# Optimization experiments

Measured on AMD Instinct MI355X. Metric: run time of the kernel, lower is better.

The kernel has to match this reference:

```python
import jax, jax.numpy as jnp
import numpy as np

NUM_USERS = 100000
USER_EMB_DIM = 64
PROC_DIM = 128          # Dense(128) embedding_processor
NUM_SHARDS = 16
MEM_SIZE = 512          # memory slots per shard
WORD_SIZE = 64
NUM_READS = 4
INPUT_SIZE = 256
B, S = 256, 128
IN_DIM = INPUT_SIZE + PROC_DIM  # combined controller input width


def setup_inputs() -> dict:
    key = jax.random.key(0)
    k = jax.random.split(key, 7)
    x = jax.random.normal(k[0], (B, S, INPUT_SIZE), dtype=jnp.float32)
    user_id = jax.random.randint(k[1], (B,), 0, NUM_USERS, dtype=jnp.int64)
    user_emb_table = jax.random.normal(k[2], (NUM_USERS, USER_EMB_DIM), dtype=jnp.float32) * 0.02
    W_proc = jax.random.normal(k[3], (USER_EMB_DIM, PROC_DIM), dtype=jnp.float32) * (1.0 / np.sqrt(USER_EMB_DIM))
    b_proc = jnp.zeros((PROC_DIM,), dtype=jnp.float32)
    # per-shard parameters: query projection + memory matrix (the shard's state)
    Wq = jax.random.normal(k[4], (NUM_SHARDS, IN_DIM, NUM_READS * WORD_SIZE), dtype=jnp.float32) * (1.0 / np.sqrt(IN_DIM))
    memory = jax.random.normal(k[5], (NUM_SHARDS, MEM_SIZE, WORD_SIZE), dtype=jnp.float32)
    return {"x": x, "user_id": user_id, "user_emb_table": user_emb_table,
            "W_proc": W_proc, "b_proc": b_proc, "Wq": Wq, "memory": memory}


def reference(x, user_id, user_emb_table, W_proc, b_proc, Wq, memory):
    # user embedding lookup + Dense processor
    ue = user_emb_table[user_id]                       # [B, E]
    pe = ue @ W_proc + b_proc                          # [B, PROC_DIM]
    # broadcast the processed embedding across the sequence and concat on features
    pe_seq = jnp.broadcast_to(pe[:, None, :], (x.shape[0], x.shape[1], pe.shape[-1]))
    combined = jnp.concatenate([x, pe_seq], axis=-1)   # [B, S, IN_DIM]
    # shard routing (irregular gather of per-shard params)
    sid = user_id % NUM_SHARDS                         # [B]
    Wq_g = Wq[sid]                                     # [B, IN_DIM, R*W]
    mem_g = memory[sid]                                # [B, M, W]
    # per-sample shard forward: content-based read
    q = jnp.einsum('bsi,bio->bso', combined, Wq_g)     # [B, S, R*W]
    q = q.reshape(q.shape[0], q.shape[1], NUM_READS, WORD_SIZE)
    scores = jnp.einsum('bsrw,bmw->bsrm', q, mem_g)    # [B, S, R, M]
    wts = jax.nn.softmax(scores, axis=-1)
    read_words = jnp.einsum('bsrm,bmw->bsrw', wts, mem_g)  # [B, S, R, W]
    # original code keeps final_states[-1] (last sample's state)
    final_state = wts[-1]                              # [S, R, M]
    return read_words, final_state
```

## Files before the change

### kernel.cpp

```cpp
#include <hip/hip_runtime.h>
#include <math.h>

#define BB 256
#define SSEQ 128
#define INPUT 256
#define PD 128
#define EE 64
#define RW 256
#define MM 512
#define WW 64
#define KD 384

typedef _Float16 half8 __attribute__((ext_vector_type(8)));
typedef __fp16 fp16x2 __attribute__((ext_vector_type(2)));
typedef float float4v __attribute__((ext_vector_type(4)));
typedef float f32x16 __attribute__((ext_vector_type(16)));
typedef unsigned int uint2v __attribute__((ext_vector_type(2)));

#define LOG2E 1.44269504088896f
#define OUT1 8388608u

#define MEMT_OFF 65536
#define MEMT16   4096
#define F32_OFF  131072
#define LDS_BYTES (131072 + 6144)
#define UE_O 0
#define PE_O 64
#define QPE_O 192
#define QP_O 448

union H8 { half8 h8; unsigned int u[4]; uint4 u4; };

__device__ __forceinline__ unsigned int pk2(float a, float b) {
    union { fp16x2 h; unsigned int u; } p;
    p.h = __builtin_amdgcn_cvt_pkrtz(a, b);
    return p.u;
}

__device__ __forceinline__ float xhalf_max(float v) {
    uint2v r = __builtin_amdgcn_permlane32_swap(__float_as_uint(v), __float_as_uint(v), false, false);
    return fmaxf(__uint_as_float(r[0]), __uint_as_float(r[1]));
}
__device__ __forceinline__ float xhalf_sum(float v) {
    uint2v r = __builtin_amdgcn_permlane32_swap(__float_as_uint(v), __float_as_uint(v), false, false);
    return __uint_as_float(r[0]) + __uint_as_float(r[1]);
}

__global__ void __launch_bounds__(1024, 4)
attn_kernel(const float* __restrict__ x, const int* __restrict__ user_id,
            const float* __restrict__ uet, const float* __restrict__ W_proc,
            const float* __restrict__ b_proc, const float* __restrict__ Wq,
            const float* __restrict__ memG, float* __restrict__ out)
{
    extern __shared__ char smraw[];
    unsigned short* smemu = (unsigned short*)smraw;
    unsigned int*   smw   = (unsigned int*)smraw;
    uint4*          sm128 = (uint4*)smraw;
    float*          smf   = (float*)(smraw + F32_OFF);

    const int t = threadIdx.x;
    const int b = blockIdx.x;
    const int lane = t & 63, wv = t >> 6;
    const int n16 = lane & 15, quad = lane >> 4;
    const int l31 = lane & 31, hh = lane >> 5;
    const int r = wv & 3, sq = wv >> 2;
    const int s0 = sq * 32;
    const int mswz = l31 & 7;

    const int uid = user_id[b];
    const int sid = uid & 15;
    const float* memB = memG + (size_t)sid * (MM*WW);
    const float* wqX  = Wq + (size_t)sid * KD * RW;

    if (t < EE) smf[UE_O + t] = uet[(size_t)uid*EE + t];

    for (int i = 0; i < 32; ++i) {
        int idx = i*1024 + t;
        int n = idx & 255, kp = idx >> 8;
        float w0 = wqX[(size_t)(2*kp)    *RW + n];
        float w1 = wqX[(size_t)(2*kp + 1)*RW + n];
        smw[((((kp>>2)*256 + n) << 2) | (kp & 3))] = pk2(w0, w1);
    }
    __syncthreads();

    if (t < PD) {
        float a = b_proc[t];
        #pragma unroll
        for (int e = 0; e < EE; ++e) a = fmaf(smf[UE_O + e], W_proc[e*PD + t], a);
        smf[PE_O + t] = a;
    }
    __syncthreads();
    {
        int n = t & 255, h = t >> 8;
        float s = 0.f;
        const float* wr = wqX + (size_t)(256 + h*32)*RW + n;
        #pragma unroll 8
        for (int k = 0; k < 32; ++k) s = fmaf(smf[PE_O + h*32 + k], wr[(size_t)k*RW], s);
        smf[QP_O + h*256 + n] = s;
    }
    __syncthreads();
    if (t < 256) smf[QPE_O + t] = LOG2E * (smf[QP_O + t] + smf[QP_O + 256 + t]
                                         + smf[QP_O + 512 + t] + smf[QP_O + 768 + t]);
    __syncthreads();

    float4v qacc[4][2];
    #pragma unroll
    for (int mt = 0; mt < 4; ++mt)
        #pragma unroll
        for (int nt = 0; nt < 2; ++nt) qacc[mt][nt] = (float4v)0.f;

    const float* xB = x + (size_t)(b*SSEQ + s0) * INPUT;
    for (int kc = 0; kc < 8; ++kc) {
        H8 afr[4];
        #pragma unroll
        for (int mt = 0; mt < 4; ++mt)
            afr[mt].u4 = sm128[(kc*4 + quad)*256 + r*64 + mt*16 + n16];
        H8 bfr[2];
        #pragma unroll
        for (int nt = 0; nt < 2; ++nt) {
            const float* xg = xB + (size_t)(nt*16 + n16)*INPUT + kc*32 + quad*8;
            float4 a0 = *(const float4*)xg;
            float4 a1 = *(const float4*)(xg + 4);
            bfr[nt].u[0] = pk2(a0.x*LOG2E, a0.y*LOG2E);
            bfr[nt].u[1] = pk2(a0.z*LOG2E, a0.w*LOG2E);
            bfr[nt].u[2] = pk2(a1.x*LOG2E, a1.y*LOG2E);
            bfr[nt].u[3] = pk2(a1.z*LOG2E, a1.w*LOG2E);
        }
        __builtin_amdgcn_s_setprio(1);
        #pragma unroll
        for (int mt = 0; mt < 4; ++mt)
            #pragma unroll
            for (int nt = 0; nt < 2; ++nt)
                qacc[mt][nt] = __builtin_amdgcn_mfma_f32_16x16x32_f16(afr[mt].h8, bfr[nt].h8, qacc[mt][nt], 0, 0, 0);
        __builtin_amdgcn_s_setprio(0);
    }
    #pragma unroll
    for (int mt = 0; mt < 4; ++mt)
        #pragma unroll
        for (int reg = 0; reg < 4; ++reg) {
            float qv = smf[QPE_O + r*64 + mt*16 + quad*4 + reg];
            #pragma unroll
            for (int nt = 0; nt < 2; ++nt) qacc[mt][nt][reg] += qv;
        }
    unsigned int pkq[4][2][2];
    #pragma unroll
    for (int mt = 0; mt < 4; ++mt)
        #pragma unroll
        for (int nt = 0; nt < 2; ++nt) {
            pkq[mt][nt][0] = pk2(qacc[mt][nt][0], qacc[mt][nt][1]);
            pkq[mt][nt][1] = pk2(qacc[mt][nt][2], qacc[mt][nt][3]);
        }
    H8 bqf[4];
    {
        const int ntSel = (lane >> 4) & 1;
        const int srcBase = (lane & 15) + (lane & 32);
        #pragma unroll
        for (int kc = 0; kc < 4; ++kc)
            #pragma unroll
            for (int jp = 0; jp < 4; ++jp) {
                const int src = srcBase + ((jp >> 1) << 4);
                int v0 = __shfl((int)pkq[kc][0][jp & 1], src, 64);
                int v1 = __shfl((int)pkq[kc][1][jp & 1], src, 64);
                bqf[kc].u[jp] = (unsigned int)(ntSel ? v1 : v0);
            }
    }
    __syncthreads();

    for (int i = 0; i < 4; ++i) {
        int id = t + i*1024;
        int m = id >> 3, cw = id & 7;
        const float* g = memB + m*64 + cw*8;
        float4 a0 = *(const float4*)g;
        float4 a1 = *(const float4*)(g + 4);
        sm128[m*8 + (cw ^ (m & 7))] =
            make_uint4(pk2(a0.x,a0.y), pk2(a0.z,a0.w), pk2(a1.x,a1.y), pk2(a1.z,a1.w));
    }
    __syncthreads();
    for (int i = 0; i < 4; ++i) {
        int id = t + i*1024;
        int w = id & 63, cm = id >> 6;
        unsigned int uu[4];
        #pragma unroll
        for (int p = 0; p < 4; ++p) {
            int m0 = cm*8 + 2*p, m1 = m0 + 1;
            unsigned short lo = smemu[m0*64 + (((w>>3) ^ (m0&7))<<3) + (w&7)];
            unsigned short hi = smemu[m1*64 + (((w>>3) ^ (m1&7))<<3) + (w&7)];
            uu[p] = (unsigned int)lo | ((unsigned int)hi << 16);
        }
        sm128[MEMT16 + w*64 + (cm ^ (w & 7))] = make_uint4(uu[0],uu[1],uu[2],uu[3]);
    }
    __syncthreads();

    f32x16 Oa0 = (f32x16)0.f, Oa1 = (f32x16)0.f;
    float Ml = -1e30f, llp = 0.f;

    H8 afc[4];
    #pragma unroll
    for (int kc = 0; kc < 4; ++kc)
        afc[kc].u4 = sm128[l31*8 + (((kc<<1) + hh) ^ mswz)];

    for (int mtile = 0; mtile < 16; ++mtile) {
        f32x16 Sa = (f32x16)0.f;
        __builtin_amdgcn_s_setprio(1);
        #pragma unroll
        for (int kc = 0; kc < 4; ++kc)
            Sa = __builtin_amdgcn_mfma_f32_32x32x16_f16(afc[kc].h8, bqf[kc].h8, Sa, 0, 0, 0);
        __builtin_amdgcn_s_setprio(0);
        if (mtile < 15) {
            const int mrow = (mtile+1)*32 + l31;
            #pragma unroll
            for (int kc = 0; kc < 4; ++kc)
                afc[kc].u4 = sm128[mrow*8 + (((kc<<1) + hh) ^ mswz)];
        }
        const int c0 = mtile*4 + hh;
        H8 afP0, afP1, afP2, afP3;
        afP0.u4 = sm128[MEMT16 + l31*64        + ( c0      ^ mswz)];
        afP1.u4 = sm128[MEMT16 + l31*64        + ((c0 + 2) ^ mswz)];
        afP2.u4 = sm128[MEMT16 + (32 + l31)*64 + ( c0      ^ mswz)];
        afP3.u4 = sm128[MEMT16 + (32 + l31)*64 + ((c0 + 2) ^ mswz)];
        float m0 = fmaxf(fmaxf(Sa[0], Sa[1]), Sa[2]);
        float m1 = fmaxf(fmaxf(Sa[3], Sa[4]), Sa[5]);
        float m2 = fmaxf(fmaxf(Sa[6], Sa[7]), Sa[8]);
        float m3 = fmaxf(fmaxf(Sa[9], Sa[10]), Sa[11]);
        float m4 = fmaxf(fmaxf(Sa[12], Sa[13]), Sa[14]);
        float m5 = fmaxf(fmaxf(m0, m1), Sa[15]);
        float m6 = fmaxf(fmaxf(m2, m3), m4);
        float tmx = xhalf_max(fmaxf(m5, m6));
        if (__any(tmx > Ml + 8.0f)) {
            float Mn = fmaxf(Ml, tmx);
            float al = __builtin_amdgcn_exp2f(Ml - Mn);
            Ml = Mn;
            llp *= al;
            #pragma unroll
            for (int g = 0; g < 16; ++g) { Oa0[g] *= al; Oa1[g] *= al; }
        }
        float pv[16];
        #pragma unroll
        for (int g = 0; g < 16; ++g) pv[g] = __builtin_amdgcn_exp2f(Sa[g] - Ml);
        float ts = (((pv[0]+pv[1])+(pv[2]+pv[3])) + ((pv[4]+pv[5])+(pv[6]+pv[7])))
                 + (((pv[8]+pv[9])+(pv[10]+pv[11])) + ((pv[12]+pv[13])+(pv[14]+pv[15])));
        llp += ts;
        uint2v rA0 = __builtin_amdgcn_permlane32_swap(pk2(pv[0],pv[1]),   pk2(pv[4],pv[5]),   false, false);
        uint2v rB0 = __builtin_amdgcn_permlane32_swap(pk2(pv[2],pv[3]),   pk2(pv[6],pv[7]),   false, false);
        uint2v rA1 = __builtin_amdgcn_permlane32_swap(pk2(pv[8],pv[9]),   pk2(pv[12],pv[13]), false, false);
        uint2v rB1 = __builtin_amdgcn_permlane32_swap(pk2(pv[10],pv[11]), pk2(pv[14],pv[15]), false, false);
        H8 bp0; bp0.u[0]=rA0[0]; bp0.u[1]=rB0[0]; bp0.u[2]=rA0[1]; bp0.u[3]=rB0[1];
        H8 bp1; bp1.u[0]=rA1[0]; bp1.u[1]=rB1[0]; bp1.u[2]=rA1[1]; bp1.u[3]=rB1[1];
        __builtin_amdgcn_s_setprio(1);
        Oa0 = __builtin_amdgcn_mfma_f32_32x32x16_f16(afP0.h8, bp0.h8, Oa0, 0, 0, 0);
        Oa0 = __builtin_amdgcn_mfma_f32_32x32x16_f16(afP1.h8, bp1.h8, Oa0, 0, 0, 0);
        Oa1 = __builtin_amdgcn_mfma_f32_32x32x16_f16(afP2.h8, bp0.h8, Oa1, 0, 0, 0);
        Oa1 = __builtin_amdgcn_mfma_f32_32x32x16_f16(afP3.h8, bp1.h8, Oa1, 0, 0, 0);
        __builtin_amdgcn_s_setprio(0);
    }

    float inv = 1.0f / xhalf_sum(llp);

    {
        const int s = s0 + l31;
        float* op = out + ((size_t)(b*SSEQ + s)*4 + r)*WW;
        #pragma unroll
        for (int rq = 0; rq < 4; ++rq) {
            float4 o0 = make_float4(Oa0[rq*4+0]*inv, Oa0[rq*4+1]*inv,
                                    Oa0[rq*4+2]*inv, Oa0[rq*4+3]*inv);
            *(float4*)&op[rq*8 + hh*4] = o0;
            float4 o1 = make_float4(Oa1[rq*4+0]*inv, Oa1[rq*4+1]*inv,
                                    Oa1[rq*4+2]*inv, Oa1[rq*4+3]*inv);
            *(float4*)&op[32 + rq*8 + hh*4] = o1;
        }
    }

    if (b == BB - 1) {
        const int s = s0 + l31;
        size_t base = (size_t)OUT1 + ((size_t)(s*4 + r) << 9);
        for (int mtile = 0; mtile < 16; ++mtile) {
            f32x16 Sa = (f32x16)0.f;
            const int mrow = mtile*32 + l31;
            #pragma unroll
            for (int kc = 0; kc < 4; ++kc) {
                H8 af; af.u4 = sm128[mrow*8 + (((kc<<1) + hh) ^ mswz)];
                Sa = __builtin_amdgcn_mfma_f32_32x32x16_f16(af.h8, bqf[kc].h8, Sa, 0, 0, 0);
            }
            #pragma unroll
            for (int rq = 0; rq < 4; ++rq) {
                float4 w4 = make_float4(
                    __builtin_amdgcn_exp2f(Sa[rq*4+0] - Ml) * inv,
                    __builtin_amdgcn_exp2f(Sa[rq*4+1] - Ml) * inv,
                    __builtin_amdgcn_exp2f(Sa[rq*4+2] - Ml) * inv,
                    __builtin_amdgcn_exp2f(Sa[rq*4+3] - Ml) * inv);
                *(float4*)&out[base + mtile*32 + rq*8 + hh*4] = w4;
            }
        }
    }
}

extern "C" void kernel_launch(void* const* d_in, const int* in_sizes, int n_in,
                              void* d_out, int out_size, void* d_ws, size_t ws_size,
                              hipStream_t stream) {
    const float* x    = (const float*)d_in[0];
    const int*   uid  = (const int*)  d_in[1];
    const float* uet  = (const float*)d_in[2];
    const float* Wp   = (const float*)d_in[3];
    const float* bp   = (const float*)d_in[4];
    const float* Wq   = (const float*)d_in[5];
    const float* mem  = (const float*)d_in[6];
    float* out = (float*)d_out;

    (void)hipFuncSetAttribute((const void*)attn_kernel,
                              hipFuncAttributeMaxDynamicSharedMemorySize, LDS_BYTES);
    attn_kernel<<<BB, 1024, LDS_BYTES, stream>>>(x, uid, uet, Wp, bp, Wq, mem, out);
}
```

Before: 165.8 us.

## Split attention into prep, query-projection and attention kernels via workspace

Adds a prep kernel that converts each shard's memory to fp16 once, in both row-major and transposed form, in global workspace. The former single kernel is split in two. The first computes the query fragments and writes them to global memory. The second loads the precomputed fp16 memory tiles directly into LDS, removing the per-block fp32 convert and LDS transpose passes and their barriers. The trade-off is two extra launches and a global round-trip of the query fragments, and it needs enough workspace, otherwise the original monolithic kernel is used.

```diff
diff --git a/kernel.cpp b/kernel.cpp
--- a/kernel.cpp
+++ b/kernel.cpp
@@ -23,12 +23,20 @@
 #define MEMT_OFF 65536
 #define MEMT16   4096
 #define F32_OFF  131072
-#define LDS_BYTES (131072 + 6144)
+#define LDS_BYTES_K1 (131072 + 6144)
+#define LDS_BYTES_K2 131072
 #define UE_O 0
 #define PE_O 64
 #define QPE_O 192
 #define QP_O 448
 
+#define QG_OFF   0u
+#define M16_OFF  (16u<<20)
+#define MT16_OFF (17u<<20)
+#define WS_NEED  (18u<<20)
+
+#define QIDX(b,r,kc,jp,hh,s) ((((((size_t)(b)*4 + (r))*4 + (kc))*4 + (jp))*2 + (hh))*128 + (s))
+
 union H8 { half8 h8; unsigned int u[4]; uint4 u4; };
 
 __device__ __forceinline__ unsigned int pk2(float a, float b) {
@@ -46,14 +54,29 @@
     return __uint_as_float(r[0]) + __uint_as_float(r[1]);
 }
 
+__global__ void __launch_bounds__(1024)
+prep_kernel(const float* __restrict__ memG, unsigned short* __restrict__ mem16,
+            unsigned short* __restrict__ memT16)
+{
+    const int sid = blockIdx.x >> 1, half = blockIdx.x & 1;
+    const size_t base = (size_t)sid * (MM*WW);
+    for (int i = 0; i < 16; ++i) {
+        int idx = half*16384 + i*1024 + threadIdx.x;
+        float f = memG[base + idx];
+        unsigned short h = (unsigned short)(pk2(f, f) & 0xFFFFu);
+        mem16[base + idx] = h;
+        int m = idx >> 6, w = idx & 63;
+        memT16[base + (size_t)w*MM + m] = h;
+    }
+}
+
 __global__ void __launch_bounds__(1024, 4)
-attn_kernel(const float* __restrict__ x, const int* __restrict__ user_id,
-            const float* __restrict__ uet, const float* __restrict__ W_proc,
-            const float* __restrict__ b_proc, const float* __restrict__ Wq,
-            const float* __restrict__ memG, float* __restrict__ out)
+attn_k1(const float* __restrict__ x, const int* __restrict__ user_id,
+        const float* __restrict__ uet, const float* __restrict__ W_proc,
+        const float* __restrict__ b_proc, const float* __restrict__ Wq,
+        unsigned int* __restrict__ qg)
 {
     extern __shared__ char smraw[];
-    unsigned short* smemu = (unsigned short*)smraw;
     unsigned int*   smw   = (unsigned int*)smraw;
     uint4*          sm128 = (uint4*)smraw;
     float*          smf   = (float*)(smraw + F32_OFF);
@@ -65,11 +88,9 @@
     const int l31 = lane & 31, hh = lane >> 5;
     const int r = wv & 3, sq = wv >> 2;
     const int s0 = sq * 32;
-    const int mswz = l31 & 7;
 
     const int uid = user_id[b];
     const int sid = uid & 15;
-    const float* memB = memG + (size_t)sid * (MM*WW);
     const float* wqX  = Wq + (size_t)sid * KD * RW;
 
     if (t < EE) smf[UE_O + t] = uet[(size_t)uid*EE + t];
@@ -164,30 +185,51 @@
                 bqf[kc].u[jp] = (unsigned int)(ntSel ? v1 : v0);
             }
     }
-    __syncthreads();
+    #pragma unroll
+    for (int kc = 0; kc < 4; ++kc)
+        #pragma unroll
+        for (int jp = 0; jp < 4; ++jp)
+            qg[QIDX(b, r, kc, jp, hh, s0 + l31)] = bqf[kc].u[jp];
+}
+
+__global__ void __launch_bounds__(1024, 4)
+attn_k2(const int* __restrict__ user_id, const unsigned short* __restrict__ mem16,
+        const unsigned short* __restrict__ memT16, const unsigned int* __restrict__ qg,
+        float* __restrict__ out)
+{
+    extern __shared__ char smraw[];
+    uint4* sm128 = (uint4*)smraw;
+
+    const int t = threadIdx.x;
+    const int b = blockIdx.x;
+    const int lane = t & 63, wv = t >> 6;
+    const int l31 = lane & 31, hh = lane >> 5;
+    const int r = wv & 3, sq = wv >> 2;
+    const int s0 = sq * 32;
+    const int mswz = l31 & 7;
+
+    const int uid = user_id[b];
+    const int sid = uid & 15;
+    const size_t mbase = (size_t)sid * (MM*WW);
+
+    H8 bqf[4];
+    #pragma unroll
+    for (int kc = 0; kc < 4; ++kc)
+        #pragma unroll
+        for (int jp = 0; jp < 4; ++jp)
+            bqf[kc].u[jp] = qg[QIDX(b, r, kc, jp, hh, s0 + l31)];
 
     for (int i = 0; i < 4; ++i) {
         int id = t + i*1024;
         int m = id >> 3, cw = id & 7;
-        const float* g = memB + m*64 + cw*8;
-        float4 a0 = *(const float4*)g;
-        float4 a1 = *(const float4*)(g + 4);
         sm128[m*8 + (cw ^ (m & 7))] =
-            make_uint4(pk2(a0.x,a0.y), pk2(a0.z,a0.w), pk2(a1.x,a1.y), pk2(a1.z,a1.w));
-    }
-    __syncthreads();
+            *(const uint4*)(mem16 + mbase + (size_t)m*64 + cw*8);
+    }
     for (int i = 0; i < 4; ++i) {
         int id = t + i*1024;
         int w = id & 63, cm = id >> 6;
-        unsigned int uu[4];
-        #pragma unroll
-        for (int p = 0; p < 4; ++p) {
-            int m0 = cm*8 + 2*p, m1 = m0 + 1;
-            unsigned short lo = smemu[m0*64 + (((w>>3) ^ (m0&7))<<3) + (w&7)];
-            unsigned short hi = smemu[m1*64 + (((w>>3) ^ (m1&7))<<3) + (w&7)];
-            uu[p] = (unsigned int)lo | ((unsigned int)hi << 16);
-        }
-        sm128[MEMT16 + w*64 + (cm ^ (w & 7))] = make_uint4(uu[0],uu[1],uu[2],uu[3]);
+        sm128[MEMT16 + w*64 + (cm ^ (w & 7))] =
+            *(const uint4*)(memT16 + mbase + (size_t)w*MM + cm*8);
     }
     __syncthreads();
 
@@ -294,6 +336,254 @@
     }
 }
 
+__global__ void __launch_bounds__(1024, 4)
+attn_kernel_mono(const float* __restrict__ x, const int* __restrict__ user_id,
+            const float* __restrict__ uet, const float* __restrict__ W_proc,
+            const float* __restrict__ b_proc, const float* __restrict__ Wq,
+            const float* __restrict__ memG, float* __restrict__ out)
+{
+    extern __shared__ char smraw[];
+    unsigned short* smemu = (unsigned short*)smraw;
+    unsigned int*   smw   = (unsigned int*)smraw;
+    uint4*          sm128 = (uint4*)smraw;
+    float*          smf   = (float*)(smraw + F32_OFF);
+
+    const int t = threadIdx.x;
+    const int b = blockIdx.x;
+    const int lane = t & 63, wv = t >> 6;
+    const int n16 = lane & 15, quad = lane >> 4;
+    const int l31 = lane & 31, hh = lane >> 5;
+    const int r = wv & 3, sq = wv >> 2;
+    const int s0 = sq * 32;
+    const int mswz = l31 & 7;
+
+    const int uid = user_id[b];
+    const int sid = uid & 15;
+    const float* memB = memG + (size_t)sid * (MM*WW);
+    const float* wqX  = Wq + (size_t)sid * KD * RW;
+
+    if (t < EE) smf[UE_O + t] = uet[(size_t)uid*EE + t];
+
+    for (int i = 0; i < 32; ++i) {
+        int idx = i*1024 + t;
+        int n = idx & 255, kp = idx >> 8;
+        float w0 = wqX[(size_t)(2*kp)    *RW + n];
+        float w1 = wqX[(size_t)(2*kp + 1)*RW + n];
+        smw[((((kp>>2)*256 + n) << 2) | (kp & 3))] = pk2(w0, w1);
+    }
+    __syncthreads();
+
+    if (t < PD) {
+        float a = b_proc[t];
+        #pragma unroll
+        for (int e = 0; e < EE; ++e) a = fmaf(smf[UE_O + e], W_proc[e*PD + t], a);
+        smf[PE_O + t] = a;
+    }
+    __syncthreads();
+    {
+        int n = t & 255, h = t >> 8;
+        float s = 0.f;
+        const float* wr = wqX + (size_t)(256 + h*32)*RW + n;
+        #pragma unroll 8
+        for (int k = 0; k < 32; ++k) s = fmaf(smf[PE_O + h*32 + k], wr[(size_t)k*RW], s);
+        smf[QP_O + h*256 + n] = s;
+    }
+    __syncthreads();
+    if (t < 256) smf[QPE_O + t] = LOG2E * (smf[QP_O + t] + smf[QP_O + 256 + t]
+                                         + smf[QP_O + 512 + t] + smf[QP_O + 768 + t]);
+    __syncthreads();
+
+    float4v qacc[4][2];
+    #pragma unroll
+    for (int mt = 0; mt < 4; ++mt)
+        #pragma unroll
+        for (int nt = 0; nt < 2; ++nt) qacc[mt][nt] = (float4v)0.f;
+
+    const float* xB = x + (size_t)(b*SSEQ + s0) * INPUT;
+    for (int kc = 0; kc < 8; ++kc) {
+        H8 afr[4];
+        #pragma unroll
+        for (int mt = 0; mt < 4; ++mt)
+            afr[mt].u4 = sm128[(kc*4 + quad)*256 + r*64 + mt*16 + n16];
+        H8 bfr[2];
+        #pragma unroll
+        for (int nt = 0; nt < 2; ++nt) {
+            const float* xg = xB + (size_t)(nt*16 + n16)*INPUT + kc*32 + quad*8;
+            float4 a0 = *(const float4*)xg;
+            float4 a1 = *(const float4*)(xg + 4);
+            bfr[nt].u[0] = pk2(a0.x*LOG2E, a0.y*LOG2E);
+            bfr[nt].u[1] = pk2(a0.z*LOG2E, a0.w*LOG2E);
+            bfr[nt].u[2] = pk2(a1.x*LOG2E, a1.y*LOG2E);
+            bfr[nt].u[3] = pk2(a1.z*LOG2E, a1.w*LOG2E);
+        }
+        __builtin_amdgcn_s_setprio(1);
+        #pragma unroll
+        for (int mt = 0; mt < 4; ++mt)
+            #pragma unroll
+            for (int nt = 0; nt < 2; ++nt)
+                qacc[mt][nt] = __builtin_amdgcn_mfma_f32_16x16x32_f16(afr[mt].h8, bfr[nt].h8, qacc[mt][nt], 0, 0, 0);
+        __builtin_amdgcn_s_setprio(0);
+    }
+    #pragma unroll
+    for (int mt = 0; mt < 4; ++mt)
+        #pragma unroll
+        for (int reg = 0; reg < 4; ++reg) {
+            float qv = smf[QPE_O + r*64 + mt*16 + quad*4 + reg];
+            #pragma unroll
+            for (int nt = 0; nt < 2; ++nt) qacc[mt][nt][reg] += qv;
+        }
+    unsigned int pkq[4][2][2];
+    #pragma unroll
+    for (int mt = 0; mt < 4; ++mt)
+        #pragma unroll
+        for (int nt = 0; nt < 2; ++nt) {
+            pkq[mt][nt][0] = pk2(qacc[mt][nt][0], qacc[mt][nt][1]);
+            pkq[mt][nt][1] = pk2(qacc[mt][nt][2], qacc[mt][nt][3]);
+        }
+    H8 bqf[4];
+    {
+        const int ntSel = (lane >> 4) & 1;
+        const int srcBase = (lane & 15) + (lane & 32);
+        #pragma unroll
+        for (int kc = 0; kc < 4; ++kc)
+            #pragma unroll
+            for (int jp = 0; jp < 4; ++jp) {
+                const int src = srcBase + ((jp >> 1) << 4);
+                int v0 = __shfl((int)pkq[kc][0][jp & 1], src, 64);
+                int v1 = __shfl((int)pkq[kc][1][jp & 1], src, 64);
+                bqf[kc].u[jp] = (unsigned int)(ntSel ? v1 : v0);
+            }
+    }
+    __syncthreads();
+
+    for (int i = 0; i < 4; ++i) {
+        int id = t + i*1024;
+        int m = id >> 3, cw = id & 7;
+        const float* g = memB + m*64 + cw*8;
+        float4 a0 = *(const float4*)g;
+        float4 a1 = *(const float4*)(g + 4);
+        sm128[m*8 + (cw ^ (m & 7))] =
+            make_uint4(pk2(a0.x,a0.y), pk2(a0.z,a0.w), pk2(a1.x,a1.y), pk2(a1.z,a1.w));
+    }
+    __syncthreads();
+    for (int i = 0; i < 4; ++i) {
+        int id = t + i*1024;
+        int w = id & 63, cm = id >> 6;
+        unsigned int uu[4];
+        #pragma unroll
+        for (int p = 0; p < 4; ++p) {
+            int m0 = cm*8 + 2*p, m1 = m0 + 1;
+            unsigned short lo = smemu[m0*64 + (((w>>3) ^ (m0&7))<<3) + (w&7)];
+            unsigned short hi = smemu[m1*64 + (((w>>3) ^ (m1&7))<<3) + (w&7)];
+            uu[p] = (unsigned int)lo | ((unsigned int)hi << 16);
+        }
+        sm128[MEMT16 + w*64 + (cm ^ (w & 7))] = make_uint4(uu[0],uu[1],uu[2],uu[3]);
+    }
+    __syncthreads();
+
+    f32x16 Oa0 = (f32x16)0.f, Oa1 = (f32x16)0.f;
+    float Ml = -1e30f, llp = 0.f;
+
+    H8 afc[4];
+    #pragma unroll
+    for (int kc = 0; kc < 4; ++kc)
+        afc[kc].u4 = sm128[l31*8 + (((kc<<1) + hh) ^ mswz)];
+
+    for (int mtile = 0; mtile < 16; ++mtile) {
+        f32x16 Sa = (f32x16)0.f;
+        __builtin_amdgcn_s_setprio(1);
+        #pragma unroll
+        for (int kc = 0; kc < 4; ++kc)
+            Sa = __builtin_amdgcn_mfma_f32_32x32x16_f16(afc[kc].h8, bqf[kc].h8, Sa, 0, 0, 0);
+        __builtin_amdgcn_s_setprio(0);
+        if (mtile < 15) {
+            const int mrow = (mtile+1)*32 + l31;
+            #pragma unroll
+            for (int kc = 0; kc < 4; ++kc)
+                afc[kc].u4 = sm128[mrow*8 + (((kc<<1) + hh) ^ mswz)];
+        }
+        const int c0 = mtile*4 + hh;
+        H8 afP0, afP1, afP2, afP3;
+        afP0.u4 = sm128[MEMT16 + l31*64        + ( c0      ^ mswz)];
+        afP1.u4 = sm128[MEMT16 + l31*64        + ((c0 + 2) ^ mswz)];
+        afP2.u4 = sm128[MEMT16 + (32 + l31)*64 + ( c0      ^ mswz)];
+        afP3.u4 = sm128[MEMT16 + (32 + l31)*64 + ((c0 + 2) ^ mswz)];
+        float m0 = fmaxf(fmaxf(Sa[0], Sa[1]), Sa[2]);
+        float m1 = fmaxf(fmaxf(Sa[3], Sa[4]), Sa[5]);
+        float m2 = fmaxf(fmaxf(Sa[6], Sa[7]), Sa[8]);
+        float m3 = fmaxf(fmaxf(Sa[9], Sa[10]), Sa[11]);
+        float m4 = fmaxf(fmaxf(Sa[12], Sa[13]), Sa[14]);
+        float m5 = fmaxf(fmaxf(m0, m1), Sa[15]);
+        float m6 = fmaxf(fmaxf(m2, m3), m4);
+        float tmx = xhalf_max(fmaxf(m5, m6));
+        if (__any(tmx > Ml + 8.0f)) {
+            float Mn = fmaxf(Ml, tmx);
+            float al = __builtin_amdgcn_exp2f(Ml - Mn);
+            Ml = Mn;
+            llp *= al;
+            #pragma unroll
+            for (int g = 0; g < 16; ++g) { Oa0[g] *= al; Oa1[g] *= al; }
+        }
+        float pv[16];
+        #pragma unroll
+        for (int g = 0; g < 16; ++g) pv[g] = __builtin_amdgcn_exp2f(Sa[g] - Ml);
+        float ts = (((pv[0]+pv[1])+(pv[2]+pv[3])) + ((pv[4]+pv[5])+(pv[6]+pv[7])))
+                 + (((pv[8]+pv[9])+(pv[10]+pv[11])) + ((pv[12]+pv[13])+(pv[14]+pv[15])));
+        llp += ts;
+        uint2v rA0 = __builtin_amdgcn_permlane32_swap(pk2(pv[0],pv[1]),   pk2(pv[4],pv[5]),   false, false);
+        uint2v rB0 = __builtin_amdgcn_permlane32_swap(pk2(pv[2],pv[3]),   pk2(pv[6],pv[7]),   false, false);
+        uint2v rA1 = __builtin_amdgcn_permlane32_swap(pk2(pv[8],pv[9]),   pk2(pv[12],pv[13]), false, false);
+        uint2v rB1 = __builtin_amdgcn_permlane32_swap(pk2(pv[10],pv[11]), pk2(pv[14],pv[15]), false, false);
+        H8 bp0; bp0.u[0]=rA0[0]; bp0.u[1]=rB0[0]; bp0.u[2]=rA0[1]; bp0.u[3]=rB0[1];
+        H8 bp1; bp1.u[0]=rA1[0]; bp1.u[1]=rB1[0]; bp1.u[2]=rA1[1]; bp1.u[3]=rB1[1];
+        __builtin_amdgcn_s_setprio(1);
+        Oa0 = __builtin_amdgcn_mfma_f32_32x32x16_f16(afP0.h8, bp0.h8, Oa0, 0, 0, 0);
+        Oa0 = __builtin_amdgcn_mfma_f32_32x32x16_f16(afP1.h8, bp1.h8, Oa0, 0, 0, 0);
+        Oa1 = __builtin_amdgcn_mfma_f32_32x32x16_f16(afP2.h8, bp0.h8, Oa1, 0, 0, 0);
+        Oa1 = __builtin_amdgcn_mfma_f32_32x32x16_f16(afP3.h8, bp1.h8, Oa1, 0, 0, 0);
+        __builtin_amdgcn_s_setprio(0);
+    }
+
+    float inv = 1.0f / xhalf_sum(llp);
+
+    {
+        const int s = s0 + l31;
+        float* op = out + ((size_t)(b*SSEQ + s)*4 + r)*WW;
+        #pragma unroll
+        for (int rq = 0; rq < 4; ++rq) {
+            float4 o0 = make_float4(Oa0[rq*4+0]*inv, Oa0[rq*4+1]*inv,
+                                    Oa0[rq*4+2]*inv, Oa0[rq*4+3]*inv);
+            *(float4*)&op[rq*8 + hh*4] = o0;
+            float4 o1 = make_float4(Oa1[rq*4+0]*inv, Oa1[rq*4+1]*inv,
+                                    Oa1[rq*4+2]*inv, Oa1[rq*4+3]*inv);
+            *(float4*)&op[32 + rq*8 + hh*4] = o1;
+        }
+    }
+
+    if (b == BB - 1) {
+        const int s = s0 + l31;
+        size_t base = (size_t)OUT1 + ((size_t)(s*4 + r) << 9);
+        for (int mtile = 0; mtile < 16; ++mtile) {
+            f32x16 Sa = (f32x16)0.f;
+            const int mrow = mtile*32 + l31;
+            #pragma unroll
+            for (int kc = 0; kc < 4; ++kc) {
+                H8 af; af.u4 = sm128[mrow*8 + (((kc<<1) + hh) ^ mswz)];
+                Sa = __builtin_amdgcn_mfma_f32_32x32x16_f16(af.h8, bqf[kc].h8, Sa, 0, 0, 0);
+            }
+            #pragma unroll
+            for (int rq = 0; rq < 4; ++rq) {
+                float4 w4 = make_float4(
+                    __builtin_amdgcn_exp2f(Sa[rq*4+0] - Ml) * inv,
+                    __builtin_amdgcn_exp2f(Sa[rq*4+1] - Ml) * inv,
+                    __builtin_amdgcn_exp2f(Sa[rq*4+2] - Ml) * inv,
+                    __builtin_amdgcn_exp2f(Sa[rq*4+3] - Ml) * inv);
+                *(float4*)&out[base + mtile*32 + rq*8 + hh*4] = w4;
+            }
+        }
+    }
+}
+
 extern "C" void kernel_launch(void* const* d_in, const int* in_sizes, int n_in,
                               void* d_out, int out_size, void* d_ws, size_t ws_size,
                               hipStream_t stream) {
@@ -306,7 +596,20 @@
     const float* mem  = (const float*)d_in[6];
     float* out = (float*)d_out;
 
-    (void)hipFuncSetAttribute((const void*)attn_kernel,
-                              hipFuncAttributeMaxDynamicSharedMemorySize, LDS_BYTES);
-    attn_kernel<<<BB, 1024, LDS_BYTES, stream>>>(x, uid, uet, Wp, bp, Wq, mem, out);
-}
+    if (ws_size >= WS_NEED && d_ws != nullptr) {
+        unsigned int*   qg     = (unsigned int*)((char*)d_ws + QG_OFF);
+        unsigned short* mem16  = (unsigned short*)((char*)d_ws + M16_OFF);
+        unsigned short* memT16 = (unsigned short*)((char*)d_ws + MT16_OFF);
+        (void)hipFuncSetAttribute((const void*)attn_k1,
+                                  hipFuncAttributeMaxDynamicSharedMemorySize, LDS_BYTES_K1);
+        (void)hipFuncSetAttribute((const void*)attn_k2,
+                                  hipFuncAttributeMaxDynamicSharedMemorySize, LDS_BYTES_K2);
+        prep_kernel<<<32, 1024, 0, stream>>>(mem, mem16, memT16);
+        attn_k1<<<BB, 1024, LDS_BYTES_K1, stream>>>(x, uid, uet, Wp, bp, Wq, qg);
+        attn_k2<<<BB, 1024, LDS_BYTES_K2, stream>>>(uid, mem16, memT16, qg, out);
+    } else {
+        (void)hipFuncSetAttribute((const void*)attn_kernel_mono,
+                                  hipFuncAttributeMaxDynamicSharedMemorySize, LDS_BYTES_K1);
+        attn_kernel_mono<<<BB, 1024, LDS_BYTES_K1, stream>>>(x, uid, uet, Wp, bp, Wq, mem, out);
+    }
+}
```

After: 187.2 us. +12.9%, slower.

## Stream Wq in double-buffered k-chunks and load memory before Q projection

Applied to the files above, without the earlier changes.

Instead of staging the whole 256-row Wq slice in LDS as fp16 before the Q projection, the kernel now streams it in 32-row chunks into a double buffer, loading the next chunk while the current one feeds the MFMAs. The memory matrix is staged into LDS first, alongside the user embedding load, so the memory layout no longer has to wait for the projection to finish. This shrinks the Wq staging footprint and the large up-front load phase, and lets global loads overlap with compute. The cost is a barrier on every k-chunk iteration and a larger LDS allocation constant.

```diff
diff --git a/kernel.cpp b/kernel.cpp
--- a/kernel.cpp
+++ b/kernel.cpp
@@ -20,10 +20,10 @@
 #define LOG2E 1.44269504088896f
 #define OUT1 8388608u
 
-#define MEMT_OFF 65536
 #define MEMT16   4096
-#define F32_OFF  131072
-#define LDS_BYTES (131072 + 6144)
+#define F32_OFF  65536
+#define BUF16    8192
+#define LDS_BYTES 163840
 #define UE_O 0
 #define PE_O 64
 #define QPE_O 192
@@ -54,7 +54,6 @@
 {
     extern __shared__ char smraw[];
     unsigned short* smemu = (unsigned short*)smraw;
-    unsigned int*   smw   = (unsigned int*)smraw;
     uint4*          sm128 = (uint4*)smraw;
     float*          smf   = (float*)(smraw + F32_OFF);
 
@@ -72,100 +71,6 @@
     const float* memB = memG + (size_t)sid * (MM*WW);
     const float* wqX  = Wq + (size_t)sid * KD * RW;
 
-    if (t < EE) smf[UE_O + t] = uet[(size_t)uid*EE + t];
-
-    for (int i = 0; i < 32; ++i) {
-        int idx = i*1024 + t;
-        int n = idx & 255, kp = idx >> 8;
-        float w0 = wqX[(size_t)(2*kp)    *RW + n];
-        float w1 = wqX[(size_t)(2*kp + 1)*RW + n];
-        smw[((((kp>>2)*256 + n) << 2) | (kp & 3))] = pk2(w0, w1);
-    }
-    __syncthreads();
-
-    if (t < PD) {
-        float a = b_proc[t];
-        #pragma unroll
-        for (int e = 0; e < EE; ++e) a = fmaf(smf[UE_O + e], W_proc[e*PD + t], a);
-        smf[PE_O + t] = a;
-    }
-    __syncthreads();
-    {
-        int n = t & 255, h = t >> 8;
-        float s = 0.f;
-        const float* wr = wqX + (size_t)(256 + h*32)*RW + n;
-        #pragma unroll 8
-        for (int k = 0; k < 32; ++k) s = fmaf(smf[PE_O + h*32 + k], wr[(size_t)k*RW], s);
-        smf[QP_O + h*256 + n] = s;
-    }
-    __syncthreads();
-    if (t < 256) smf[QPE_O + t] = LOG2E * (smf[QP_O + t] + smf[QP_O + 256 + t]
-                                         + smf[QP_O + 512 + t] + smf[QP_O + 768 + t]);
-    __syncthreads();
-
-    float4v qacc[4][2];
-    #pragma unroll
-    for (int mt = 0; mt < 4; ++mt)
-        #pragma unroll
-        for (int nt = 0; nt < 2; ++nt) qacc[mt][nt] = (float4v)0.f;
-
-    const float* xB = x + (size_t)(b*SSEQ + s0) * INPUT;
-    for (int kc = 0; kc < 8; ++kc) {
-        H8 afr[4];
-        #pragma unroll
-        for (int mt = 0; mt < 4; ++mt)
-            afr[mt].u4 = sm128[(kc*4 + quad)*256 + r*64 + mt*16 + n16];
-        H8 bfr[2];
-        #pragma unroll
-        for (int nt = 0; nt < 2; ++nt) {
-            const float* xg = xB + (size_t)(nt*16 + n16)*INPUT + kc*32 + quad*8;
-            float4 a0 = *(const float4*)xg;
-            float4 a1 = *(const float4*)(xg + 4);
-            bfr[nt].u[0] = pk2(a0.x*LOG2E, a0.y*LOG2E);
-            bfr[nt].u[1] = pk2(a0.z*LOG2E, a0.w*LOG2E);
-            bfr[nt].u[2] = pk2(a1.x*LOG2E, a1.y*LOG2E);
-            bfr[nt].u[3] = pk2(a1.z*LOG2E, a1.w*LOG2E);
-        }
-        __builtin_amdgcn_s_setprio(1);
-        #pragma unroll
-        for (int mt = 0; mt < 4; ++mt)
-            #pragma unroll
-            for (int nt = 0; nt < 2; ++nt)
-                qacc[mt][nt] = __builtin_amdgcn_mfma_f32_16x16x32_f16(afr[mt].h8, bfr[nt].h8, qacc[mt][nt], 0, 0, 0);
-        __builtin_amdgcn_s_setprio(0);
-    }
-    #pragma unroll
-    for (int mt = 0; mt < 4; ++mt)
-        #pragma unroll
-        for (int reg = 0; reg < 4; ++reg) {
-            float qv = smf[QPE_O + r*64 + mt*16 + quad*4 + reg];
-            #pragma unroll
-            for (int nt = 0; nt < 2; ++nt) qacc[mt][nt][reg] += qv;
-        }
-    unsigned int pkq[4][2][2];
-    #pragma unroll
-    for (int mt = 0; mt < 4; ++mt)
-        #pragma unroll
-        for (int nt = 0; nt < 2; ++nt) {
-            pkq[mt][nt][0] = pk2(qacc[mt][nt][0], qacc[mt][nt][1]);
-            pkq[mt][nt][1] = pk2(qacc[mt][nt][2], qacc[mt][nt][3]);
-        }
-    H8 bqf[4];
-    {
-        const int ntSel = (lane >> 4) & 1;
-        const int srcBase = (lane & 15) + (lane & 32);
-        #pragma unroll
-        for (int kc = 0; kc < 4; ++kc)
-            #pragma unroll
-            for (int jp = 0; jp < 4; ++jp) {
-                const int src = srcBase + ((jp >> 1) << 4);
-                int v0 = __shfl((int)pkq[kc][0][jp & 1], src, 64);
-                int v1 = __shfl((int)pkq[kc][1][jp & 1], src, 64);
-                bqf[kc].u[jp] = (unsigned int)(ntSel ? v1 : v0);
-            }
-    }
-    __syncthreads();
-
     for (int i = 0; i < 4; ++i) {
         int id = t + i*1024;
         int m = id >> 3, cw = id & 7;
@@ -175,7 +80,116 @@
         sm128[m*8 + (cw ^ (m & 7))] =
             make_uint4(pk2(a0.x,a0.y), pk2(a0.z,a0.w), pk2(a1.x,a1.y), pk2(a1.z,a1.w));
     }
-    __syncthreads();
+    if (t < EE) smf[UE_O + t] = uet[(size_t)uid*EE + t];
+    __syncthreads();
+
+    if (t < PD) {
+        float a = b_proc[t];
+        #pragma unroll
+        for (int e = 0; e < EE; ++e) a = fmaf(smf[UE_O + e], W_proc[e*PD + t], a);
+        smf[PE_O + t] = a;
+    }
+    __syncthreads();
+    {
+        int n = t & 255, h = t >> 8;
+        float s = 0.f;
+        const float* wr = wqX + (size_t)(256 + h*32)*RW + n;
+        #pragma unroll 8
+        for (int k = 0; k < 32; ++k) s = fmaf(smf[PE_O + h*32 + k], wr[(size_t)k*RW], s);
+        smf[QP_O + h*256 + n] = s;
+    }
+    __syncthreads();
+    if (t < 256) smf[QPE_O + t] = LOG2E * (smf[QP_O + t] + smf[QP_O + 256 + t]
+                                         + smf[QP_O + 512 + t] + smf[QP_O + 768 + t]);
+    __syncthreads();
+
+    {
+        int kq = t >> 8, n = t & 255;
+        const float* wr = wqX + (size_t)(kq*8)*RW + n;
+        float w0 = wr[0*RW], w1 = wr[1*RW], w2 = wr[2*RW], w3 = wr[3*RW];
+        float w4 = wr[4*RW], w5 = wr[5*RW], w6 = wr[6*RW], w7 = wr[7*RW];
+        sm128[BUF16 + kq*256 + n] =
+            make_uint4(pk2(w0,w1), pk2(w2,w3), pk2(w4,w5), pk2(w6,w7));
+    }
+    __syncthreads();
+
+    float4v qacc[4][2];
+    #pragma unroll
+    for (int mt = 0; mt < 4; ++mt)
+        #pragma unroll
+        for (int nt = 0; nt < 2; ++nt) qacc[mt][nt] = (float4v)0.f;
+
+    const float* xB = x + (size_t)(b*SSEQ + s0) * INPUT;
+    for (int kc = 0; kc < 8; ++kc) {
+        float4 xlo[2], xhi[2];
+        #pragma unroll
+        for (int nt = 0; nt < 2; ++nt) {
+            const float* xg = xB + (size_t)(nt*16 + n16)*INPUT + kc*32 + quad*8;
+            xlo[nt] = *(const float4*)xg;
+            xhi[nt] = *(const float4*)(xg + 4);
+        }
+        if (kc < 7) {
+            int c = kc + 1;
+            int kq = t >> 8, n = t & 255;
+            const float* wr = wqX + (size_t)(c*32 + kq*8)*RW + n;
+            float w0 = wr[0*RW], w1 = wr[1*RW], w2 = wr[2*RW], w3 = wr[3*RW];
+            float w4 = wr[4*RW], w5 = wr[5*RW], w6 = wr[6*RW], w7 = wr[7*RW];
+            sm128[BUF16 + (c&1)*1024 + kq*256 + n] =
+                make_uint4(pk2(w0,w1), pk2(w2,w3), pk2(w4,w5), pk2(w6,w7));
+        }
+        H8 afr[4];
+        #pragma unroll
+        for (int mt = 0; mt < 4; ++mt)
+            afr[mt].u4 = sm128[BUF16 + (kc&1)*1024 + quad*256 + r*64 + mt*16 + n16];
+        H8 bfr[2];
+        #pragma unroll
+        for (int nt = 0; nt < 2; ++nt) {
+            bfr[nt].u[0] = pk2(xlo[nt].x*LOG2E, xlo[nt].y*LOG2E);
+            bfr[nt].u[1] = pk2(xlo[nt].z*LOG2E, xlo[nt].w*LOG2E);
+            bfr[nt].u[2] = pk2(xhi[nt].x*LOG2E, xhi[nt].y*LOG2E);
+            bfr[nt].u[3] = pk2(xhi[nt].z*LOG2E, xhi[nt].w*LOG2E);
+        }
+        __builtin_amdgcn_s_setprio(1);
+        #pragma unroll
+        for (int mt = 0; mt < 4; ++mt)
+            #pragma unroll
+            for (int nt = 0; nt < 2; ++nt)
+                qacc[mt][nt] = __builtin_amdgcn_mfma_f32_16x16x32_f16(afr[mt].h8, bfr[nt].h8, qacc[mt][nt], 0, 0, 0);
+        __builtin_amdgcn_s_setprio(0);
+        __syncthreads();
+    }
+    #pragma unroll
+    for (int mt = 0; mt < 4; ++mt)
+        #pragma unroll
+        for (int reg = 0; reg < 4; ++reg) {
+            float qv = smf[QPE_O + r*64 + mt*16 + quad*4 + reg];
+            #pragma unroll
+            for (int nt = 0; nt < 2; ++nt) qacc[mt][nt][reg] += qv;
+        }
+    unsigned int pkq[4][2][2];
+    #pragma unroll
+    for (int mt = 0; mt < 4; ++mt)
+        #pragma unroll
+        for (int nt = 0; nt < 2; ++nt) {
+            pkq[mt][nt][0] = pk2(qacc[mt][nt][0], qacc[mt][nt][1]);
+            pkq[mt][nt][1] = pk2(qacc[mt][nt][2], qacc[mt][nt][3]);
+        }
+    H8 bqf[4];
+    {
+        const int ntSel = (lane >> 4) & 1;
+        const int srcBase = (lane & 15) + (lane & 32);
+        #pragma unroll
+        for (int kc = 0; kc < 4; ++kc)
+            #pragma unroll
+            for (int jp = 0; jp < 4; ++jp) {
+                const int src = srcBase + ((jp >> 1) << 4);
+                int v0 = __shfl((int)pkq[kc][0][jp & 1], src, 64);
+                int v1 = __shfl((int)pkq[kc][1][jp & 1], src, 64);
+                bqf[kc].u[jp] = (unsigned int)(ntSel ? v1 : v0);
+            }
+    }
+    __syncthreads();
+
     for (int i = 0; i < 4; ++i) {
         int id = t + i*1024;
         int w = id & 63, cm = id >> 6;
```

Result: slower. 169.4 us (+2.2%).
